# Kernel optimization log

Hardware: AMD Instinct MI355X
Metric: run time of the kernel (lower is better)

The kernel has to match this reference:

```python
import jax, jax.numpy as jnp
import numpy as np
import math

D_MODEL, N_HEADS, DK, DV, D_FF, GROUP_KV, GW = 1024, 16, 64, 64, 4096, 4, 16
EPS = 1e-6

def _rms(x, w):
    # RMSNorm over last dim: x * rsqrt(mean(x^2)+eps) * weight
    return x * jax.lax.rsqrt(jnp.mean(x * x, axis=-1, keepdims=True) + EPS) * w

def setup_inputs() -> dict:
    key = jax.random.key(0)
    ks = jax.random.split(key, 12)
    s = lambda k, shape, scale: (jax.random.normal(k, shape, dtype=jnp.float32) * scale)
    return {
        "x": s(ks[0], (2, 2048, D_MODEL), 1.0),
        "norm_in_w": jnp.ones((D_MODEL,), jnp.float32),
        "gw": s(ks[1], (GW, D_MODEL), 0.02),
        "Wq": s(ks[2], (D_MODEL, N_HEADS * DK), 1.0 / math.sqrt(D_MODEL)),
        "Wk": s(ks[3], (D_MODEL, GROUP_KV * DK), 1.0 / math.sqrt(D_MODEL)),
        "Wv": s(ks[4], (D_MODEL, GROUP_KV * DV), 1.0 / math.sqrt(D_MODEL)),
        "Wo": s(ks[5], (N_HEADS * DV, D_MODEL), 1.0 / math.sqrt(N_HEADS * DV)),
        "head_norm_w": jnp.ones((N_HEADS, DV), jnp.float32),
        "ff_norm_w": jnp.ones((D_MODEL,), jnp.float32),
        "W1": s(ks[6], (D_MODEL, D_FF), 1.0 / math.sqrt(D_MODEL)),
        "W3": s(ks[7], (D_MODEL, D_FF), 1.0 / math.sqrt(D_MODEL)),
        "W2": s(ks[8], (D_FF, D_MODEL), 1.0 / math.sqrt(D_FF)),
    }

def reference(x, norm_in_w, gw, Wq, Wk, Wv, Wo, head_norm_w, ff_norm_w, W1, W3, W2):
    b, seq, d = x.shape
    R = N_HEADS // GROUP_KV  # heads per kv group
    h = _rms(x, norm_in_w)
    # prepend global workspace tokens
    h = jnp.concatenate([jnp.broadcast_to(gw[None], (b, GW, d)), h], axis=1)
    t = h.shape[1]
    q = (h @ Wq).reshape(b, t, N_HEADS, DK)
    k = jnp.repeat((h @ Wk).reshape(b, t, GROUP_KV, DK), R, axis=2)  # [b,t,H,dk]
    v = jnp.repeat((h @ Wv).reshape(b, t, GROUP_KV, DV), R, axis=2)  # [b,t,H,dv]
    scores = jnp.einsum("bqhd,bkhd->bhqk", q, k) / math.sqrt(DK)
    causal = jnp.arange(t)[:, None] >= jnp.arange(t)[None, :]
    scores = jnp.where(causal[None, None], scores, -jnp.inf)
    weights = jax.nn.softmax(scores, axis=-1)
    ctx = jnp.einsum("bhqk,bkhd->bqhd", weights, v)  # [b,t,H,dv]
    # headwise RMSNorm over dv with per-head weight
    ctx = ctx * jax.lax.rsqrt(jnp.mean(ctx * ctx, axis=-1, keepdims=True) + EPS)
    ctx = ctx * head_norm_w[None, None]
    ctx = ctx.reshape(b, t, N_HEADS * DV)[:, GW:]  # drop gw token outputs
    y = x + ctx @ Wo
    z = _rms(y, ff_norm_w)
    y = y + (jax.nn.silu(z @ W1) * (z @ W3)) @ W2
    return y
```

## Files before the change

### kernel.cpp

```cpp
#include <hip/hip_runtime.h>

typedef unsigned short u16;
typedef __attribute__((ext_vector_type(8))) _Float16 f16x8;
typedef __attribute__((ext_vector_type(4))) float f32x4;

#define TPB 2064
#define NROW 4128
#define VTS 2080

__device__ __forceinline__ u16 f2h(float f) {
    _Float16 h = (_Float16)f;
    return __builtin_bit_cast(u16, h);
}
__device__ __forceinline__ float h2f(u16 u) {
    return (float)__builtin_bit_cast(_Float16, u);
}
__device__ __forceinline__ float wave_sum(float v) {
    #pragma unroll
    for (int m = 32; m; m >>= 1) v += __shfl_xor(v, m, 64);
    return v;
}
__device__ __forceinline__ void gl_lds16(const u16* g, u16* l) {
    __builtin_amdgcn_global_load_lds((const __attribute__((address_space(1))) void*)g,
                                     (__attribute__((address_space(3))) void*)l, 16, 0, 0);
}

__global__ __launch_bounds__(256) void wconv_t_kernel(const float* __restrict__ src,
                                                      u16* __restrict__ dst, int K, int N) {
    __shared__ float tile[32][33];
    const int k0 = blockIdx.y * 32, n0 = blockIdx.x * 32;
    const int tx = threadIdx.x & 31, ty0 = threadIdx.x >> 5;
    #pragma unroll
    for (int r = 0; r < 4; r++) {
        int ky = ty0 + r * 8;
        tile[ky][tx] = src[(size_t)(k0 + ky) * N + n0 + tx];
    }
    __syncthreads();
    #pragma unroll
    for (int r = 0; r < 4; r++) {
        int ny = ty0 + r * 8;
        dst[(size_t)(n0 + ny) * K + k0 + tx] = f2h(tile[tx][ny]);
    }
}

__global__ __launch_bounds__(256) void vtrans_kernel(const u16* __restrict__ qkv,
                                                     u16* __restrict__ vt) {
    __shared__ u16 tile[32][33];
    const int bg = blockIdx.z;
    const int b = bg >> 2, g = bg & 3;
    const int t0 = blockIdx.x * 32, d0 = blockIdx.y * 32;
    const int tx = threadIdx.x & 31, ty0 = threadIdx.x >> 5;
    #pragma unroll
    for (int r = 0; r < 4; r++) {
        int t = t0 + ty0 + r * 8;
        u16 v = 0;
        if (t < TPB) v = qkv[(size_t)(b * TPB + t) * 1536 + 1280 + g * 64 + d0 + tx];
        tile[ty0 + r * 8][tx] = v;
    }
    __syncthreads();
    #pragma unroll
    for (int r = 0; r < 4; r++) {
        int d = d0 + ty0 + r * 8;
        vt[((size_t)bg * 64 + d) * VTS + t0 + tx] = tile[tx][ty0 + r * 8];
    }
}

__global__ __launch_bounds__(256) void rms_in_kernel(const float* __restrict__ x,
                                                     const float* __restrict__ w,
                                                     const float* __restrict__ gwp,
                                                     u16* __restrict__ h) {
    const int r = blockIdx.x;
    const int b = r / TPB, pos = r - b * TPB;
    const int tid = threadIdx.x;
    u16* hr = h + (size_t)r * 1024;
    if (pos < 16) {
        const float* s = gwp + (size_t)pos * 1024;
        for (int c = tid; c < 1024; c += 256) hr[c] = f2h(s[c]);
        return;
    }
    const float* xr = x + ((size_t)b * 2048 + (pos - 16)) * 1024;
    float v[4]; float ss = 0.f;
    #pragma unroll
    for (int i = 0; i < 4; i++) { v[i] = xr[tid + 256 * i]; ss += v[i] * v[i]; }
    ss = wave_sum(ss);
    __shared__ float red[4];
    if ((tid & 63) == 0) red[tid >> 6] = ss;
    __syncthreads();
    float tot = red[0] + red[1] + red[2] + red[3];
    float rn = rsqrtf(tot * (1.f / 1024.f) + 1e-6f);
    #pragma unroll
    for (int i = 0; i < 4; i++) hr[tid + 256 * i] = f2h(v[i] * rn * w[tid + 256 * i]);
}

__global__ __launch_bounds__(256) void rms_row_kernel(const float* __restrict__ in,
                                                      const float* __restrict__ w,
                                                      u16* __restrict__ out) {
    const int r = blockIdx.x;
    const int tid = threadIdx.x;
    const float* xr = in + (size_t)r * 1024;
    float v[4]; float ss = 0.f;
    #pragma unroll
    for (int i = 0; i < 4; i++) { v[i] = xr[tid + 256 * i]; ss += v[i] * v[i]; }
    ss = wave_sum(ss);
    __shared__ float red[4];
    if ((tid & 63) == 0) red[tid >> 6] = ss;
    __syncthreads();
    float tot = red[0] + red[1] + red[2] + red[3];
    float rn = rsqrtf(tot * (1.f / 1024.f) + 1e-6f);
    u16* orow = out + (size_t)r * 1024;
    #pragma unroll
    for (int i = 0; i < 4; i++) orow[tid + 256 * i] = f2h(v[i] * rn * w[tid + 256 * i]);
}

__device__ __forceinline__ void stage_tile(const u16* __restrict__ A, const u16* __restrict__ B,
                                           u16* As, u16* Bs, int m0, int n0, int k0,
                                           int M, int K, int tid) {
    const int wb = tid & ~63;
    #pragma unroll
    for (int t = 0; t < 2; t++) {
        int seg = t * 256 + tid;
        int row = seg >> 2, kc = seg & 3;
        int ar = m0 + row; if (ar > M - 1) ar = M - 1;
        gl_lds16(A + (size_t)ar * K + k0 + kc * 8, As + (size_t)(t * 256 + wb) * 8);
        gl_lds16(B + (size_t)(n0 + row) * K + k0 + kc * 8, Bs + (size_t)(t * 256 + wb) * 8);
    }
}

template <int EPI>
__global__ __launch_bounds__(256, 2) void gemm_bt(const u16* __restrict__ A,
                                                  const u16* __restrict__ B,
                                                  void* Cout,
                                                  const void* aux,
                                                  int M, int N, int K) {
    __shared__ __align__(16) u16 As[2][4096];
    __shared__ __align__(16) u16 Bs[2][4096];
    const int tid = threadIdx.x;
    const int m0 = blockIdx.y * 128, n0 = blockIdx.x * 128;
    const int w = tid >> 6, l = tid & 63;
    const int wr = w >> 1, wc = w & 1, lr = l & 15, lg = l >> 4;
    f32x4 acc[4][4] = {};
    const int NT = K >> 5;
    stage_tile(A, B, As[0], Bs[0], m0, n0, 0, M, K, tid);
    for (int t = 0; t < NT; t++) {
        const int p = t & 1;
        __syncthreads();
        if (t + 1 < NT) stage_tile(A, B, As[p ^ 1], Bs[p ^ 1], m0, n0, (t + 1) * 32, M, K, tid);
        f16x8 af[4], bf[4];
        #pragma unroll
        for (int i = 0; i < 4; i++) {
            af[i] = *(const f16x8*)&As[p][(wr * 64 + i * 16 + lr) * 32 + lg * 8];
            bf[i] = *(const f16x8*)&Bs[p][(wc * 64 + i * 16 + lr) * 32 + lg * 8];
        }
        #pragma unroll
        for (int i = 0; i < 4; i++)
            #pragma unroll
            for (int j = 0; j < 4; j++)
                acc[i][j] = __builtin_amdgcn_mfma_f32_16x16x32_f16(af[i], bf[j], acc[i][j], 0, 0, 0);
    }
    #pragma unroll
    for (int i = 0; i < 4; i++) {
        const int rowb = m0 + wr * 64 + i * 16 + lg * 4;
        #pragma unroll
        for (int j = 0; j < 4; j++) {
            const int col = n0 + wc * 64 + j * 16 + lr;
            #pragma unroll
            for (int e = 0; e < 4; e++) {
                const int r2 = rowb + e;
                if (r2 < M) {
                    const size_t idx = (size_t)r2 * N + col;
                    const float v = acc[i][j][e];
                    if constexpr (EPI == 0) {
                        ((u16*)Cout)[idx] = f2h(v);
                    } else if constexpr (EPI == 1) {
                        ((float*)Cout)[idx] = v + ((const float*)aux)[idx];
                    } else {
                        float t0 = h2f(((const u16*)aux)[idx]);
                        float s = t0 / (1.f + __expf(-t0));
                        ((u16*)Cout)[idx] = f2h(s * v);
                    }
                }
            }
        }
    }
}

__global__ __launch_bounds__(256) void attn_kernel(const u16* __restrict__ qkv,
                                                   const u16* __restrict__ vt,
                                                   u16* __restrict__ ctxn,
                                                   const float* __restrict__ hnw) {
    __shared__ __align__(16) u16 Ks[2][2048];
    __shared__ __align__(16) u16 Vs[2][2048];
    const int bx = blockIdx.x, g = blockIdx.y, b = blockIdx.z;
    const int tid = threadIdx.x;
    const int w = tid >> 6, l = tid & 63;
    const int lr = l & 15, lg = l >> 4;
    const int h = g * 4 + w;
    const int sig = 8 * (lr >> 2) + (lr & 3);
    const int LASTROW = TPB - 1;
    const u16* vtb = vt + (size_t)(b * 4 + g) * 64 * VTS;
    const u16* kbase = qkv + (size_t)b * TPB * 1536 + 1024 + g * 64;

    const int krow = tid >> 3;
    const int ksrc = (tid & 7) ^ ((krow & 3) | (((krow >> 3) & 1) << 2));
    const int vdv = tid >> 2;
    const int vsrc = (tid & 3) ^ ((vdv >> 1) & 3);
    const int wb8 = (tid & ~63) * 8;

    const int swzr = (sig & 3) | (((sig >> 3) & 1) << 2);
    const int ka0  = sig * 64 + ((lg ^ swzr) << 3);
    const int ka0b = sig * 64 + (((lg + 4) ^ swzr) << 3);
    const int ka1  = (sig + 4) * 64 + ((lg ^ swzr) << 3);
    const int ka1b = (sig + 4) * 64 + (((lg + 4) ^ swzr) << 3);
    int kv_off[4];
    #pragma unroll
    for (int dt = 0; dt < 4; dt++) {
        const int dv = dt * 16 + lr;
        kv_off[dt] = dv * 32 + ((lg ^ ((dv >> 1) & 3)) << 3);
    }

    const float hw0 = hnw[h * 64 + 0 * 16 + lr];
    const float hw1 = hnw[h * 64 + 1 * 16 + lr];
    const float hw2 = hnw[h * 64 + 2 * 16 + lr];
    const float hw3 = hnw[h * 64 + 3 * 16 + lr];

    for (int half = 0; half < 2; half++) {
        const int qt = half ? (127 - bx) : bx;
        const int orow0 = qt * 16;
        const int qpos0 = 16 + orow0;
        const int qpos = qpos0 + lr;
        const u16* qbase = qkv + (size_t)(b * TPB + qpos) * 1536 + h * 64;
        const f16x8 qf0 = *(const f16x8*)(qbase + lg * 8);
        const f16x8 qf1 = *(const f16x8*)(qbase + 32 + lg * 8);

        float m = -INFINITY, lsum = 0.f;
        f32x4 oc[4] = {};
        const int NT = ((qpos0 + 15) >> 5) + 1;

        __syncthreads();
        gl_lds16(kbase + (size_t)krow * 1536 + ksrc * 8, Ks[0] + wb8);
        gl_lds16(vtb + (size_t)vdv * VTS + vsrc * 8, Vs[0] + wb8);

        for (int kt = 0; kt < NT; kt++) {
            const int p = kt & 1;
            const int kb = kt * 32;
            __syncthreads();
            if (kt + 1 < NT) {
                const int kb2 = kb + 32;
                int kr = kb2 + krow; if (kr > LASTROW) kr = LASTROW;
                gl_lds16(kbase + (size_t)kr * 1536 + ksrc * 8, Ks[p ^ 1] + wb8);
                gl_lds16(vtb + (size_t)vdv * VTS + kb2 + vsrc * 8, Vs[p ^ 1] + wb8);
            }
            const f16x8 a0  = *(const f16x8*)&Ks[p][ka0];
            const f16x8 a0b = *(const f16x8*)&Ks[p][ka0b];
            const f16x8 a1  = *(const f16x8*)&Ks[p][ka1];
            const f16x8 a1b = *(const f16x8*)&Ks[p][ka1b];
            f16x8 vf[4];
            #pragma unroll
            for (int dt = 0; dt < 4; dt++) vf[dt] = *(const f16x8*)&Vs[p][kv_off[dt]];

            f32x4 st0 = {}, st1 = {};
            st0 = __builtin_amdgcn_mfma_f32_16x16x32_f16(a0,  qf0, st0, 0, 0, 0);
            st0 = __builtin_amdgcn_mfma_f32_16x16x32_f16(a0b, qf1, st0, 0, 0, 0);
            st1 = __builtin_amdgcn_mfma_f32_16x16x32_f16(a1,  qf0, st1, 0, 0, 0);
            st1 = __builtin_amdgcn_mfma_f32_16x16x32_f16(a1b, qf1, st1, 0, 0, 0);

            float sv[8]; float bm = -INFINITY;
            if (kb + 31 <= qpos0) {
                #pragma unroll
                for (int j = 0; j < 4; j++) {
                    sv[j] = st0[j] * 0.125f;
                    sv[4 + j] = st1[j] * 0.125f;
                    bm = fmaxf(bm, fmaxf(sv[j], sv[4 + j]));
                }
            } else {
                #pragma unroll
                for (int j = 0; j < 4; j++) {
                    const int kva = kb + 8 * lg + j;
                    float s0 = st0[j] * 0.125f; if (kva > qpos) s0 = -INFINITY;
                    float s1 = st1[j] * 0.125f; if (kva + 4 > qpos) s1 = -INFINITY;
                    sv[j] = s0; sv[4 + j] = s1;
                    bm = fmaxf(bm, fmaxf(s0, s1));
                }
            }
            bm = fmaxf(bm, __shfl_xor(bm, 16, 64));
            bm = fmaxf(bm, __shfl_xor(bm, 32, 64));
            if (!__all(bm - m <= 8.f)) {
                const float nm = fmaxf(m, bm);
                const float sc = __expf(m - nm);
                m = nm;
                lsum *= sc;
                float scj[4];
                #pragma unroll
                for (int j = 0; j < 4; j++) scj[j] = __shfl(sc, 4 * lg + j, 64);
                #pragma unroll
                for (int dt = 0; dt < 4; dt++)
                    #pragma unroll
                    for (int j = 0; j < 4; j++) oc[dt][j] *= scj[j];
            }
            float ps = 0.f;
            f16x8 pa;
            #pragma unroll
            for (int j = 0; j < 8; j++) {
                float p2 = __expf(sv[j] - m);
                ps += p2;
                pa[j] = (_Float16)p2;
            }
            ps += __shfl_xor(ps, 16, 64); ps += __shfl_xor(ps, 32, 64);
            lsum += ps;
            #pragma unroll
            for (int dt = 0; dt < 4; dt++)
                oc[dt] = __builtin_amdgcn_mfma_f32_16x16x32_f16(pa, vf[dt], oc[dt], 0, 0, 0);
        }
        float lj[4];
        #pragma unroll
        for (int j = 0; j < 4; j++) lj[j] = __shfl(lsum, 4 * lg + j, 64);
        float o[4][4]; float ssq[4] = {0, 0, 0, 0};
        #pragma unroll
        for (int dt = 0; dt < 4; dt++)
            #pragma unroll
            for (int j = 0; j < 4; j++) {
                float v = oc[dt][j] / lj[j];
                o[dt][j] = v; ssq[j] += v * v;
            }
        float rj[4];
        #pragma unroll
        for (int j = 0; j < 4; j++) {
            float s = ssq[j];
            s += __shfl_xor(s, 1, 64); s += __shfl_xor(s, 2, 64);
            s += __shfl_xor(s, 4, 64); s += __shfl_xor(s, 8, 64);
            rj[j] = rsqrtf(s * (1.f / 64.f) + 1e-6f);
        }
        const float hwv[4] = {hw0, hw1, hw2, hw3};
        #pragma unroll
        for (int dt = 0; dt < 4; dt++) {
            #pragma unroll
            for (int j = 0; j < 4; j++) {
                const int orow = orow0 + 4 * lg + j;
                ctxn[(size_t)(b * 2048 + orow) * 1024 + h * 64 + dt * 16 + lr] =
                    f2h(o[dt][j] * rj[j] * hwv[dt]);
            }
        }
    }
}

extern "C" void kernel_launch(void* const* d_in, const int* in_sizes, int n_in,
                              void* d_out, int out_size, void* d_ws, size_t ws_size,
                              hipStream_t stream) {
    const float* x   = (const float*)d_in[0];
    const float* wn  = (const float*)d_in[1];
    const float* gw  = (const float*)d_in[2];
    const float* Wq  = (const float*)d_in[3];
    const float* Wk  = (const float*)d_in[4];
    const float* Wv  = (const float*)d_in[5];
    const float* Wo  = (const float*)d_in[6];
    const float* hnw = (const float*)d_in[7];
    const float* wf  = (const float*)d_in[8];
    const float* W1  = (const float*)d_in[9];
    const float* W3  = (const float*)d_in[10];
    const float* W2  = (const float*)d_in[11];

    char* ws = (char*)d_ws;
    u16*  wqkv = (u16*)(ws + 0);
    u16*  wo_t = (u16*)(ws + 3145728);
    u16*  w1t  = (u16*)(ws + 5242880);
    u16*  w3t  = (u16*)(ws + 13631488);
    u16*  w2t  = (u16*)(ws + 22020096);
    u16*  hbuf = (u16*)(ws + 30408704);
    u16*  qkvb = (u16*)(ws + 38862848);
    u16*  ctxn = hbuf;
    float* yb  = (float*)(ws + 51544064);
    u16*  zb   = (u16*)(ws + 68321280);
    u16*  g1   = (u16*)(ws + 76709888);
    u16*  vt   = (u16*)(ws + 110264320);
    float* outp = (float*)d_out;

    const dim3 blk(256);
    wconv_t_kernel<<<dim3(32, 32), blk, 0, stream>>>(Wq, wqkv, 1024, 1024);
    wconv_t_kernel<<<dim3(8, 32), blk, 0, stream>>>(Wk, wqkv + 1024 * 1024, 1024, 256);
    wconv_t_kernel<<<dim3(8, 32), blk, 0, stream>>>(Wv, wqkv + 1280 * 1024, 1024, 256);
    wconv_t_kernel<<<dim3(32, 32), blk, 0, stream>>>(Wo, wo_t, 1024, 1024);
    wconv_t_kernel<<<dim3(128, 32), blk, 0, stream>>>(W1, w1t, 1024, 4096);
    wconv_t_kernel<<<dim3(128, 32), blk, 0, stream>>>(W3, w3t, 1024, 4096);
    wconv_t_kernel<<<dim3(32, 128), blk, 0, stream>>>(W2, w2t, 4096, 1024);

    rms_in_kernel<<<dim3(NROW), blk, 0, stream>>>(x, wn, gw, hbuf);
    gemm_bt<0><<<dim3(12, 33), blk, 0, stream>>>(hbuf, wqkv, qkvb, nullptr, NROW, 1536, 1024);
    vtrans_kernel<<<dim3(65, 2, 8), blk, 0, stream>>>(qkvb, vt);
    attn_kernel<<<dim3(64, 4, 2), blk, 0, stream>>>(qkvb, vt, ctxn, hnw);
    gemm_bt<1><<<dim3(8, 32), blk, 0, stream>>>(ctxn, wo_t, yb, x, 4096, 1024, 1024);
    rms_row_kernel<<<dim3(4096), blk, 0, stream>>>(yb, wf, zb);
    gemm_bt<0><<<dim3(32, 32), blk, 0, stream>>>(zb, w1t, g1, nullptr, 4096, 4096, 1024);
    gemm_bt<2><<<dim3(32, 32), blk, 0, stream>>>(zb, w3t, g1, g1, 4096, 4096, 1024);
    gemm_bt<1><<<dim3(8, 32), blk, 0, stream>>>(g1, w2t, outp, yb, 4096, 1024, 4096);
}
```

Baseline: 368.7 us.

## Fuse W1/W3 GEMMs into one interleaved GEMM with SwiGLU epilogue, add XCD swizzle

Packs W1 and W3 into a single interleaved transposed weight matrix, 16 columns of each per 32-column block, so one GEMM produces both the gate and up projections in the same tile and applies silu(a)*b in the epilogue. This removes the separate W3 GEMM pass, the f16 round trip of the gate activations through g1, and a second read of zb. It also adds a block-index remap that spreads consecutive workgroups across the 8 XCDs, with an optional column-major ordering, to improve L2 locality. The fused epilogue computes the gate from the unrounded fp32 accumulator, which changes numerics slightly.

Measured after the change: 345.7 us. 1.07x faster.

```diff
diff --git a/kernel.cpp b/kernel.cpp
--- a/kernel.cpp
+++ b/kernel.cpp
@@ -40,6 +40,30 @@
     for (int r = 0; r < 4; r++) {
         int ny = ty0 + r * 8;
         dst[(size_t)(n0 + ny) * K + k0 + tx] = f2h(tile[tx][ny]);
+    }
+}
+
+__global__ __launch_bounds__(256) void wconv_pack13_kernel(const float* __restrict__ W1,
+                                                           const float* __restrict__ W3,
+                                                           u16* __restrict__ dst) {
+    __shared__ float t1[32][33];
+    __shared__ float t3[32][33];
+    const int f0 = blockIdx.x * 32, k0 = blockIdx.y * 32;
+    const int tx = threadIdx.x & 31, ty0 = threadIdx.x >> 5;
+    #pragma unroll
+    for (int r = 0; r < 4; r++) {
+        int ky = ty0 + r * 8;
+        t1[ky][tx] = W1[(size_t)(k0 + ky) * 4096 + f0 + tx];
+        t3[ky][tx] = W3[(size_t)(k0 + ky) * 4096 + f0 + tx];
+    }
+    __syncthreads();
+    #pragma unroll
+    for (int r = 0; r < 4; r++) {
+        int fy = ty0 + r * 8;
+        int f = f0 + fy;
+        int p1 = (f >> 4) * 32 + (f & 15);
+        dst[(size_t)p1 * 1024 + k0 + tx] = f2h(t1[tx][fy]);
+        dst[(size_t)(p1 + 16) * 1024 + k0 + tx] = f2h(t3[tx][fy]);
     }
 }
 
@@ -131,11 +155,23 @@
                                                   const u16* __restrict__ B,
                                                   void* Cout,
                                                   const void* aux,
-                                                  int M, int N, int K) {
+                                                  int M, int N, int K, int swzmode) {
     __shared__ __align__(16) u16 As[2][4096];
     __shared__ __align__(16) u16 Bs[2][4096];
     const int tid = threadIdx.x;
-    const int m0 = blockIdx.y * 128, n0 = blockIdx.x * 128;
+    const int gx = gridDim.x, gy = gridDim.y;
+    const int nwg = gx * gy;
+    int lid = swzmode ? (blockIdx.x * gy + blockIdx.y) : (blockIdx.y * gx + blockIdx.x);
+    {
+        const int q = nwg >> 3, rr = nwg & 7;
+        const int xc = lid & 7, o = lid >> 3;
+        lid = (xc < rr ? xc * (q + 1) : rr * (q + 1) + (xc - rr) * q) + o;
+    }
+    int bxs, bys;
+    if (swzmode) { bxs = lid / gy; bys = lid - bxs * gy; }
+    else         { bys = lid / gx; bxs = lid - bys * gx; }
+    const int m0 = bys * 128, n0 = bxs * 128;
+
     const int w = tid >> 6, l = tid & 63;
     const int wr = w >> 1, wc = w & 1, lr = l & 15, lg = l >> 4;
     f32x4 acc[4][4] = {};
@@ -157,26 +193,39 @@
             for (int j = 0; j < 4; j++)
                 acc[i][j] = __builtin_amdgcn_mfma_f32_16x16x32_f16(af[i], bf[j], acc[i][j], 0, 0, 0);
     }
-    #pragma unroll
-    for (int i = 0; i < 4; i++) {
-        const int rowb = m0 + wr * 64 + i * 16 + lg * 4;
-        #pragma unroll
-        for (int j = 0; j < 4; j++) {
-            const int col = n0 + wc * 64 + j * 16 + lr;
+    if constexpr (EPI == 3) {
+        const int ldc = N >> 1;
+        const int ucol0 = ((n0 + wc * 64) >> 1) + lr;
+        #pragma unroll
+        for (int i = 0; i < 4; i++) {
+            const int rowb = m0 + wr * 64 + i * 16 + lg * 4;
             #pragma unroll
             for (int e = 0; e < 4; e++) {
                 const int r2 = rowb + e;
-                if (r2 < M) {
-                    const size_t idx = (size_t)r2 * N + col;
-                    const float v = acc[i][j][e];
-                    if constexpr (EPI == 0) {
-                        ((u16*)Cout)[idx] = f2h(v);
-                    } else if constexpr (EPI == 1) {
-                        ((float*)Cout)[idx] = v + ((const float*)aux)[idx];
-                    } else {
-                        float t0 = h2f(((const u16*)aux)[idx]);
-                        float s = t0 / (1.f + __expf(-t0));
-                        ((u16*)Cout)[idx] = f2h(s * v);
+                const float a0 = acc[i][0][e], a1 = acc[i][1][e];
+                const float b0 = acc[i][2][e], b1 = acc[i][3][e];
+                ((u16*)Cout)[(size_t)r2 * ldc + ucol0] = f2h(a0 / (1.f + __expf(-a0)) * a1);
+                ((u16*)Cout)[(size_t)r2 * ldc + ucol0 + 16] = f2h(b0 / (1.f + __expf(-b0)) * b1);
+            }
+        }
+    } else {
+        #pragma unroll
+        for (int i = 0; i < 4; i++) {
+            const int rowb = m0 + wr * 64 + i * 16 + lg * 4;
+            #pragma unroll
+            for (int j = 0; j < 4; j++) {
+                const int col = n0 + wc * 64 + j * 16 + lr;
+                #pragma unroll
+                for (int e = 0; e < 4; e++) {
+                    const int r2 = rowb + e;
+                    if (r2 < M) {
+                        const size_t idx = (size_t)r2 * N + col;
+                        const float v = acc[i][j][e];
+                        if constexpr (EPI == 0) {
+                            ((u16*)Cout)[idx] = f2h(v);
+                        } else {
+                            ((float*)Cout)[idx] = v + ((const float*)aux)[idx];
+                        }
                     }
                 }
             }
@@ -362,8 +411,7 @@
     char* ws = (char*)d_ws;
     u16*  wqkv = (u16*)(ws + 0);
     u16*  wo_t = (u16*)(ws + 3145728);
-    u16*  w1t  = (u16*)(ws + 5242880);
-    u16*  w3t  = (u16*)(ws + 13631488);
+    u16*  w13t = (u16*)(ws + 5242880);
     u16*  w2t  = (u16*)(ws + 22020096);
     u16*  hbuf = (u16*)(ws + 30408704);
     u16*  qkvb = (u16*)(ws + 38862848);
@@ -379,17 +427,15 @@
     wconv_t_kernel<<<dim3(8, 32), blk, 0, stream>>>(Wk, wqkv + 1024 * 1024, 1024, 256);
     wconv_t_kernel<<<dim3(8, 32), blk, 0, stream>>>(Wv, wqkv + 1280 * 1024, 1024, 256);
     wconv_t_kernel<<<dim3(32, 32), blk, 0, stream>>>(Wo, wo_t, 1024, 1024);
-    wconv_t_kernel<<<dim3(128, 32), blk, 0, stream>>>(W1, w1t, 1024, 4096);
-    wconv_t_kernel<<<dim3(128, 32), blk, 0, stream>>>(W3, w3t, 1024, 4096);
+    wconv_pack13_kernel<<<dim3(128, 32), blk, 0, stream>>>(W1, W3, w13t);
     wconv_t_kernel<<<dim3(32, 128), blk, 0, stream>>>(W2, w2t, 4096, 1024);
 
     rms_in_kernel<<<dim3(NROW), blk, 0, stream>>>(x, wn, gw, hbuf);
-    gemm_bt<0><<<dim3(12, 33), blk, 0, stream>>>(hbuf, wqkv, qkvb, nullptr, NROW, 1536, 1024);
+    gemm_bt<0><<<dim3(12, 33), blk, 0, stream>>>(hbuf, wqkv, qkvb, nullptr, NROW, 1536, 1024, 0);
     vtrans_kernel<<<dim3(65, 2, 8), blk, 0, stream>>>(qkvb, vt);
     attn_kernel<<<dim3(64, 4, 2), blk, 0, stream>>>(qkvb, vt, ctxn, hnw);
-    gemm_bt<1><<<dim3(8, 32), blk, 0, stream>>>(ctxn, wo_t, yb, x, 4096, 1024, 1024);
+    gemm_bt<1><<<dim3(8, 32), blk, 0, stream>>>(ctxn, wo_t, yb, x, 4096, 1024, 1024, 0);
     rms_row_kernel<<<dim3(4096), blk, 0, stream>>>(yb, wf, zb);
-    gemm_bt<0><<<dim3(32, 32), blk, 0, stream>>>(zb, w1t, g1, nullptr, 4096, 4096, 1024);
-    gemm_bt<2><<<dim3(32, 32), blk, 0, stream>>>(zb, w3t, g1, g1, 4096, 4096, 1024);
-    gemm_bt<1><<<dim3(8, 32), blk, 0, stream>>>(g1, w2t, outp, yb, 4096, 1024, 4096);
-}
+    gemm_bt<3><<<dim3(64, 32), blk, 0, stream>>>(zb, w13t, g1, nullptr, 4096, 8192, 1024, 1);
+    gemm_bt<1><<<dim3(8, 32), blk, 0, stream>>>(g1, w2t, outp, yb, 4096, 1024, 4096, 0);
+}
```
